# Kernel optimization log

Measured on AMD Instinct MI355X. Metric: run time of the kernel, lower is better.

Reference implementation:

```python
import jax, jax.numpy as jnp
import numpy as np

PATCH_GRID = 28          # _embed hard-codes reshape(28, 28, D)
TARGET_HW = (224, 224)   # input_shape[-2:] for RescaleSegmentor


def setup_inputs() -> dict:
    key = jax.random.key(0)
    k1, k2 = jax.random.split(key)
    B = 8
    D = 1536          # 768 (CLS) + 768 (patch token) concat from DINO vitb8
    N_BANK = 50000    # coreset memory bank size
    features = jax.random.normal(k1, (B * PATCH_GRID * PATCH_GRID, D), dtype=jnp.float32)
    memory_bank = jax.random.normal(k2, (N_BANK, D), dtype=jnp.float32)
    return {"features": features, "memory_bank": memory_bank, "batchsize": B}


def reference(features, memory_bank, batchsize):
    # FaissNN IndexFlatL2 with k=1: min squared-L2 distance per query.
    # d2[i,j] = ||q_i||^2 + ||b_j||^2 - 2 q_i . b_j
    qn = jnp.sum(features * features, axis=-1, keepdims=True)          # [Q,1]
    bn = jnp.sum(memory_bank * memory_bank, axis=-1)                   # [N]
    d2 = qn + bn[None, :] - 2.0 * (features @ memory_bank.T)           # [Q,N]
    patch_scores = jnp.min(d2, axis=-1)                                # [Q] (k=1 -> mean of 1 NN)
    # unpatch_scores + PatchMaker.score: max over patches per image
    patch_maps = patch_scores.reshape(batchsize, PATCH_GRID, PATCH_GRID)
    image_scores = jnp.max(patch_maps.reshape(batchsize, -1), axis=-1)  # [B]
    # RescaleSegmentor: bilinear upsample of patch score map to input size
    masks = jax.image.resize(
        patch_maps, (batchsize, TARGET_HW[0], TARGET_HW[1]), method="linear"
    )
    return image_scores, masks
```

## Files before the change

### kernel.cpp

```cpp
#include <hip/hip_runtime.h>
#include <stdint.h>

#define DIM   1536
#define NQ    6272
#define NQP   6400
#define NB    50000
#define NBP2  50176
#define MT3   50
#define NT3   196
#define GRID3 (MT3 * NT3)
#define NPIX  (8 * 224 * 224)

typedef float f32x4 __attribute__((ext_vector_type(4)));
typedef int   i32x4 __attribute__((ext_vector_type(4)));
typedef __attribute__((address_space(3))) signed char lds_i8;

__device__ inline void gll16(const signed char* g, signed char* l) {
  __builtin_amdgcn_global_load_lds(
      (const __attribute__((address_space(1))) uint32_t*)g,
      (__attribute__((address_space(3))) uint32_t*)l, 16, 0, 0);
}

__global__ void init_kernel(uint32_t* __restrict__ minbits, float* __restrict__ out_scores) {
  int i = blockIdx.x * 256 + threadIdx.x;
  if (i < NQP) minbits[i] = 0x7F800000u;
  if (i < 8)   out_scores[i] = 0.0f;
}

__global__ void quant_rows(const float* __restrict__ src, signed char* __restrict__ dst,
                           float* __restrict__ norms, float* __restrict__ scales,
                           int nsrc, int ndst) {
  int row  = blockIdx.x * 4 + (threadIdx.x >> 6);
  int lane = threadIdx.x & 63;
  if (row >= ndst) return;
  uint32_t* drow = (uint32_t*)(dst + (size_t)row * DIM);
  if (row < nsrc) {
    const float4* s = (const float4*)(src + (size_t)row * DIM);
    float4 v[6]; float ns = 0.f, mx = 0.f;
#pragma unroll
    for (int i = 0; i < 6; ++i) {
      v[i] = s[lane + 64 * i];
      ns += v[i].x * v[i].x + v[i].y * v[i].y + v[i].z * v[i].z + v[i].w * v[i].w;
      mx = fmaxf(mx, fmaxf(fmaxf(fabsf(v[i].x), fabsf(v[i].y)),
                           fmaxf(fabsf(v[i].z), fabsf(v[i].w))));
    }
#pragma unroll
    for (int off = 32; off >= 1; off >>= 1) {
      ns += __shfl_xor(ns, off);
      mx = fmaxf(mx, __shfl_xor(mx, off));
    }
    float inv = (mx > 0.f) ? 127.0f / mx : 0.f;
#pragma unroll
    for (int i = 0; i < 6; ++i) {
      int a = max(-127, min(127, __float2int_rn(v[i].x * inv)));
      int b = max(-127, min(127, __float2int_rn(v[i].y * inv)));
      int c = max(-127, min(127, __float2int_rn(v[i].z * inv)));
      int d = max(-127, min(127, __float2int_rn(v[i].w * inv)));
      drow[lane + 64 * i] = (uint32_t)(a & 255) | ((uint32_t)(b & 255) << 8) |
                            ((uint32_t)(c & 255) << 16) | ((uint32_t)(d & 255) << 24);
    }
    if (lane == 0) { norms[row] = ns; scales[row] = mx * (1.0f / 127.0f); }
  } else {
#pragma unroll
    for (int i = 0; i < 6; ++i) drow[lane + 64 * i] = 0u;
    if (lane == 0) { norms[row] = 1e30f; scales[row] = 0.f; }
  }
}

#define BAR   do { asm volatile("s_barrier" ::: "memory"); \
                   __builtin_amdgcn_sched_barrier(0); } while(0)
#define LGKM0 do { asm volatile("s_waitcnt lgkmcnt(0)" ::: "memory"); \
                   __builtin_amdgcn_sched_barrier(0); } while(0)
#define VM0   asm volatile("s_waitcnt vmcnt(0)" ::: "memory")
#define VM3   asm volatile("s_waitcnt vmcnt(3)" ::: "memory")
#define NOGATE
#define PHI   __builtin_amdgcn_s_setprio(1)
#define PLO   __builtin_amdgcn_s_setprio(0)

#define DSR(dst, base, imm) \
  asm volatile("ds_read_b128 %0, %1 offset:%2" : "=v"(dst) : "v"(base), "i"(imm))

#define MFMA16 do { \
  _Pragma("unroll") for (int m_ = 0; m_ < 4; ++m_) \
  _Pragma("unroll") for (int n_ = 0; n_ < 4; ++n_) \
    acc[m_][n_] = __builtin_amdgcn_mfma_i32_16x16x64_i8( \
      __builtin_bit_cast(i32x4, a[m_]), __builtin_bit_cast(i32x4, b[n_]), \
      acc[m_][n_], 0, 0, 0); \
} while(0)

#define STAGE_AB(sb, ktc) do { \
  gll16(gA + gOffA + (ktc), &sA[sb][sdst]); \
  const signed char* _g = gB + gOffA + (ktc); \
  gll16(_g,                      &sB[sb][sdst]); \
  gll16(_g + (size_t)128 * DIM,  &sB[sb][8192 + sdst]); \
} while(0)

#define PH(buf, SN, sb, ktc, GATE) do { \
  DSR(a[0], aOff, (buf) * 8192 + 0);    DSR(a[1], aOff, (buf) * 8192 + 1024); \
  DSR(a[2], aOff, (buf) * 8192 + 2048); DSR(a[3], aOff, (buf) * 8192 + 3072); \
  DSR(b[0], bOff, (buf) * 16384 + 0);    DSR(b[1], bOff, (buf) * 16384 + 1024); \
  DSR(b[2], bOff, (buf) * 16384 + 2048); DSR(b[3], bOff, (buf) * 16384 + 3072); \
  LGKM0; \
  if (SN) STAGE_AB(sb, ktc); \
  GATE; BAR; PHI; MFMA16; PLO; \
} while(0)

__global__ __launch_bounds__(512, 4)
void gemm_min8(const signed char* __restrict__ fA, const signed char* __restrict__ bB,
               const float* __restrict__ bn, const float* __restrict__ bscale,
               const float* __restrict__ qscale, uint32_t* __restrict__ minbits) {
  __shared__ __align__(16) signed char sA[3][8192];
  __shared__ __align__(16) signed char sB[3][16384];

  const int nwg = GRID3;
  int bid = blockIdx.x;
  const int qch = nwg >> 3, rch = nwg & 7;
  int xcd = bid & 7, loc = bid >> 3;
  int swz = (xcd < rch ? xcd * (qch + 1) : rch * (qch + 1) + (xcd - rch) * qch) + loc;
  int mt = swz % MT3;
  int nt = swz / MT3;

  int tid = threadIdx.x;
  int lane = tid & 63, wave = tid >> 6;
  int wm = wave >> 2, wn = wave & 3;
  int lr = lane & 15, k16 = lane >> 4;

  const signed char* gA = fA + (size_t)(mt * 128) * DIM;
  const signed char* gB = bB + (size_t)(nt * 256) * DIM;

  size_t gOffA = (size_t)(tid >> 2) * DIM + ((tid & 3) ^ ((tid >> 3) & 3)) * 16;
  int sdst = tid * 16;

  int cxA = (k16 ^ ((lr >> 1) & 3)) * 16;
  uint32_t aOff = (uint32_t)(uintptr_t)(lds_i8*)&sA[0][(wm * 64 + lr) * 64 + cxA];
  uint32_t bOff = (uint32_t)(uintptr_t)(lds_i8*)&sB[0][(wn * 64 + lr) * 64 + cxA];

  i32x4 acc[4][4] = {};
  f32x4 a[4], b[4];

  STAGE_AB(0, 0);
  STAGE_AB(1, 64);
  VM3; BAR;

#pragma unroll 1
  for (int j = 0; j < 7; ++j) {
    int kb = j * 192;
    PH(0, 1, 2, kb + 128, VM3);
    PH(1, 1, 0, kb + 192, VM3);
    PH(2, 1, 1, kb + 256, VM3);
  }
  PH(0, 1, 2, 1472, VM3);
  PH(1, 0, 0, 0, VM0);
  PH(2, 0, 0, 0, NOGATE);

  float bnv[4], bsv[4];
#pragma unroll
  for (int n_ = 0; n_ < 4; ++n_) {
    int col = nt * 256 + wn * 64 + n_ * 16 + lr;
    bnv[n_] = bn[col];
    bsv[n_] = 2.0f * bscale[col];
  }
  int qbase = mt * 128 + wm * 64;
#pragma unroll
  for (int m_ = 0; m_ < 4; ++m_) {
    f32x4 sq = *(const f32x4*)&qscale[qbase + m_ * 16 + (lane >> 4) * 4];
#pragma unroll
    for (int r = 0; r < 4; ++r) {
      float sqr = sq[r];
      float v =          bnv[0] - bsv[0] * sqr * (float)acc[m_][0][r];
      v = fminf(v, bnv[1] - bsv[1] * sqr * (float)acc[m_][1][r]);
      v = fminf(v, bnv[2] - bsv[2] * sqr * (float)acc[m_][2][r]);
      v = fminf(v, bnv[3] - bsv[3] * sqr * (float)acc[m_][3][r]);
      v = fminf(v, __shfl_xor(v, 1));
      v = fminf(v, __shfl_xor(v, 2));
      v = fminf(v, __shfl_xor(v, 4));
      v = fminf(v, __shfl_xor(v, 8));
      if (lr == 0) {
        int q = qbase + m_ * 16 + (lane >> 4) * 4 + r;
        atomicMin(&minbits[q], __float_as_uint(v));
      }
    }
  }
}

__global__ void scores_kernel(const uint32_t* __restrict__ minbits, const float* __restrict__ qn,
                              float* __restrict__ ps, float* __restrict__ img) {
  int q = blockIdx.x * 256 + threadIdx.x;
  if (q >= NQ) return;
  float s = __uint_as_float(minbits[q]) + qn[q];
  ps[q] = s;
  atomicMax((uint32_t*)&img[q / 784], __float_as_uint(s));
}

__global__ void resize_kernel(const float* __restrict__ ps, float* __restrict__ masks) {
  int idx = blockIdx.x * 256 + threadIdx.x;
  if (idx >= NPIX) return;
  int b   = idx / (224 * 224);
  int rem = idx - b * (224 * 224);
  int oy  = rem / 224;
  int ox  = rem - oy * 224;
  float sy = (oy + 0.5f) * 0.125f - 0.5f;
  float sx = (ox + 0.5f) * 0.125f - 0.5f;
  float fy0 = floorf(sy), fx0 = floorf(sx);
  int y0 = (int)fy0, x0 = (int)fx0;
  float fy = sy - fy0, fx = sx - fx0;
  int y0c = min(max(y0, 0), 27),     y1c = min(max(y0 + 1, 0), 27);
  int x0c = min(max(x0, 0), 27),     x1c = min(max(x0 + 1, 0), 27);
  const float* p = ps + b * 784;
  float top = p[y0c * 28 + x0c] * (1.f - fx) + p[y0c * 28 + x1c] * fx;
  float bot = p[y1c * 28 + x0c] * (1.f - fx) + p[y1c * 28 + x1c] * fx;
  masks[idx] = top * (1.f - fy) + bot * fy;
}

extern "C" void kernel_launch(void* const* d_in, const int* in_sizes, int n_in,
                              void* d_out, int out_size, void* d_ws, size_t ws_size,
                              hipStream_t stream) {
  const float* features = (const float*)d_in[0];
  const float* bank     = (const float*)d_in[1];

  char* ws = (char*)d_ws;
  size_t off = 0;
  signed char* bankQ = (signed char*)(ws + off); off += (size_t)NBP2 * DIM;
  signed char* featQ = (signed char*)(ws + off); off += (size_t)NQP * DIM;
  float*    bn      = (float*)(ws + off);    off += (size_t)NBP2 * 4;
  float*    qn      = (float*)(ws + off);    off += (size_t)NQP * 4;
  float*    bscale  = (float*)(ws + off);    off += (size_t)NBP2 * 4;
  float*    qscale  = (float*)(ws + off);    off += (size_t)NQP * 4;
  uint32_t* minbits = (uint32_t*)(ws + off); off += (size_t)NQP * 4;
  float*    ps      = (float*)(ws + off);    off += (size_t)NQ * 4;

  float* out_scores = (float*)d_out;
  float* masks      = out_scores + 8;

  hipLaunchKernelGGL(init_kernel, dim3(25), dim3(256), 0, stream, minbits, out_scores);
  hipLaunchKernelGGL(quant_rows, dim3(NBP2 / 4), dim3(256), 0, stream, bank, bankQ, bn, bscale, NB, NBP2);
  hipLaunchKernelGGL(quant_rows, dim3(NQP / 4), dim3(256), 0, stream, features, featQ, qn, qscale, NQ, NQP);
  hipLaunchKernelGGL(gemm_min8, dim3(GRID3), dim3(512), 0, stream, featQ, bankQ, bn, bscale, qscale, minbits);
  hipLaunchKernelGGL(scores_kernel, dim3(25), dim3(256), 0, stream, minbits, qn, ps, out_scores);
  hipLaunchKernelGGL(resize_kernel, dim3((NPIX + 255) / 256), dim3(256), 0, stream, ps, masks);
}
```

Before: 673.0 us.

## Load A fragments directly from global into registers, dropping A LDS staging

```diff
diff --git a/kernel.cpp b/kernel.cpp
--- a/kernel.cpp
+++ b/kernel.cpp
@@ -72,7 +72,8 @@
 #define LGKM0 do { asm volatile("s_waitcnt lgkmcnt(0)" ::: "memory"); \
                    __builtin_amdgcn_sched_barrier(0); } while(0)
 #define VM0   asm volatile("s_waitcnt vmcnt(0)" ::: "memory")
-#define VM3   asm volatile("s_waitcnt vmcnt(3)" ::: "memory")
+#define VM4   asm volatile("s_waitcnt vmcnt(4)" ::: "memory")
+#define VM6   asm volatile("s_waitcnt vmcnt(6)" ::: "memory")
 #define NOGATE
 #define PHI   __builtin_amdgcn_s_setprio(1)
 #define PLO   __builtin_amdgcn_s_setprio(0)
@@ -80,36 +81,40 @@
 #define DSR(dst, base, imm) \
   asm volatile("ds_read_b128 %0, %1 offset:%2" : "=v"(dst) : "v"(base), "i"(imm))
 
-#define MFMA16 do { \
+#define GLDA(bank, u1) do { \
+  const signed char* _gp = gA + (u1) * 64; \
+  asm volatile("global_load_dwordx4 %0, %1, %2" : "=v"(bank[0]) : "v"(vofA[0]), "s"(_gp)); \
+  asm volatile("global_load_dwordx4 %0, %1, %2" : "=v"(bank[1]) : "v"(vofA[1]), "s"(_gp)); \
+  asm volatile("global_load_dwordx4 %0, %1, %2" : "=v"(bank[2]) : "v"(vofA[2]), "s"(_gp)); \
+  asm volatile("global_load_dwordx4 %0, %1, %2" : "=v"(bank[3]) : "v"(vofA[3]), "s"(_gp)); \
+} while(0)
+
+#define MFMA16(av) do { \
   _Pragma("unroll") for (int m_ = 0; m_ < 4; ++m_) \
   _Pragma("unroll") for (int n_ = 0; n_ < 4; ++n_) \
     acc[m_][n_] = __builtin_amdgcn_mfma_i32_16x16x64_i8( \
-      __builtin_bit_cast(i32x4, a[m_]), __builtin_bit_cast(i32x4, b[n_]), \
+      __builtin_bit_cast(i32x4, av[m_]), __builtin_bit_cast(i32x4, b[n_]), \
       acc[m_][n_], 0, 0, 0); \
 } while(0)
 
-#define STAGE_AB(sb, ktc) do { \
-  gll16(gA + gOffA + (ktc), &sA[sb][sdst]); \
-  const signed char* _g = gB + gOffA + (ktc); \
+#define STAGE_B(sb, ktc) do { \
+  const signed char* _g = gB + gOffB + (ktc); \
   gll16(_g,                      &sB[sb][sdst]); \
   gll16(_g + (size_t)128 * DIM,  &sB[sb][8192 + sdst]); \
 } while(0)
 
-#define PH(buf, SN, sb, ktc, GATE) do { \
-  DSR(a[0], aOff, (buf) * 8192 + 0);    DSR(a[1], aOff, (buf) * 8192 + 1024); \
-  DSR(a[2], aOff, (buf) * 8192 + 2048); DSR(a[3], aOff, (buf) * 8192 + 3072); \
+#define PH(buf, AC, AN, u1, SN, SB, KT, GATE) do { \
+  GLDA(AN, u1); \
   DSR(b[0], bOff, (buf) * 16384 + 0);    DSR(b[1], bOff, (buf) * 16384 + 1024); \
   DSR(b[2], bOff, (buf) * 16384 + 2048); DSR(b[3], bOff, (buf) * 16384 + 3072); \
-  LGKM0; \
-  if (SN) STAGE_AB(sb, ktc); \
-  GATE; BAR; PHI; MFMA16; PLO; \
+  if (SN) STAGE_B(SB, KT); \
+  LGKM0; GATE; BAR; PHI; MFMA16(AC); PLO; \
 } while(0)
 
 __global__ __launch_bounds__(512, 4)
 void gemm_min8(const signed char* __restrict__ fA, const signed char* __restrict__ bB,
                const float* __restrict__ bn, const float* __restrict__ bscale,
                const float* __restrict__ qscale, uint32_t* __restrict__ minbits) {
-  __shared__ __align__(16) signed char sA[3][8192];
   __shared__ __align__(16) signed char sB[3][16384];
 
   const int nwg = GRID3;
@@ -128,30 +133,45 @@
   const signed char* gA = fA + (size_t)(mt * 128) * DIM;
   const signed char* gB = bB + (size_t)(nt * 256) * DIM;
 
-  size_t gOffA = (size_t)(tid >> 2) * DIM + ((tid & 3) ^ ((tid >> 3) & 3)) * 16;
+  size_t gOffB = (size_t)(tid >> 2) * DIM + ((tid & 3) ^ ((tid >> 3) & 3)) * 16;
   int sdst = tid * 16;
 
-  int cxA = (k16 ^ ((lr >> 1) & 3)) * 16;
-  uint32_t aOff = (uint32_t)(uintptr_t)(lds_i8*)&sA[0][(wm * 64 + lr) * 64 + cxA];
-  uint32_t bOff = (uint32_t)(uintptr_t)(lds_i8*)&sB[0][(wn * 64 + lr) * 64 + cxA];
+  int cxB = (k16 ^ ((lr >> 1) & 3)) * 16;
+  uint32_t bOff = (uint32_t)(uintptr_t)(lds_i8*)&sB[0][(wn * 64 + lr) * 64 + cxB];
+
+  uint32_t vofA[4];
+#pragma unroll
+  for (int m_ = 0; m_ < 4; ++m_)
+    vofA[m_] = (uint32_t)((wm * 64 + m_ * 16 + lr) * DIM + k16 * 16);
 
   i32x4 acc[4][4] = {};
-  f32x4 a[4], b[4];
-
-  STAGE_AB(0, 0);
-  STAGE_AB(1, 64);
-  VM3; BAR;
+  f32x4 aE[4], aO[4], b[4];
+
+  STAGE_B(0, 0);
+  STAGE_B(1, 64);
+  GLDA(aE, 0);
+  VM6; BAR;
 
 #pragma unroll 1
-  for (int j = 0; j < 7; ++j) {
-    int kb = j * 192;
-    PH(0, 1, 2, kb + 128, VM3);
-    PH(1, 1, 0, kb + 192, VM3);
-    PH(2, 1, 1, kb + 256, VM3);
-  }
-  PH(0, 1, 2, 1472, VM3);
-  PH(1, 0, 0, 0, VM0);
-  PH(2, 0, 0, 0, NOGATE);
+  for (int j = 0; j < 3; ++j) {
+    int u = j * 6, kb = j * 384;
+    PH(0, aE, aO, u + 1, 1, 2, kb + 128, VM6);
+    PH(1, aO, aE, u + 2, 1, 0, kb + 192, VM6);
+    PH(2, aE, aO, u + 3, 1, 1, kb + 256, VM6);
+    PH(0, aO, aE, u + 4, 1, 2, kb + 320, VM6);
+    PH(1, aE, aO, u + 5, 1, 0, kb + 384, VM6);
+    PH(2, aO, aE, u + 6, 1, 1, kb + 448, VM6);
+  }
+  PH(0, aE, aO, 19, 1, 2, 1280, VM6);
+  PH(1, aO, aE, 20, 1, 0, 1344, VM6);
+  PH(2, aE, aO, 21, 1, 1, 1408, VM6);
+  PH(0, aO, aE, 22, 1, 2, 1472, VM6);
+  PH(1, aE, aO, 23, 0, 0, 0,    VM4);
+  {
+    DSR(b[0], bOff, 2 * 16384 + 0);    DSR(b[1], bOff, 2 * 16384 + 1024);
+    DSR(b[2], bOff, 2 * 16384 + 2048); DSR(b[3], bOff, 2 * 16384 + 3072);
+    LGKM0; VM0; BAR; PHI; MFMA16(aO); PLO;
+  }
 
   float bnv[4], bsv[4];
 #pragma unroll
```

New measurement: 1.240 ms. +84.3%, slower.
